# Kernel tuning notes

Measured on AMD Instinct MI355X. Metric: run time of the kernel, lower is better.

Reference implementation:

```python
import jax, jax.numpy as jnp
import numpy as np


def setup_inputs() -> dict:
    key = jax.random.key(0)
    k1, k2, k3 = jax.random.split(key, 3)
    B, Cin, H, W = 32, 128, 56, 56
    E, Cout = 8, 128
    x = jax.random.normal(k1, (B, Cin, H, W), dtype=jnp.float32)
    conv_w = jax.random.normal(k2, (E, Cout, Cin, 3, 3), dtype=jnp.float32) * 0.05
    gate_w = jax.random.normal(k3, (E, Cin), dtype=jnp.float32) * 0.05
    gate_b = jnp.zeros((E,), dtype=jnp.float32)
    return {"x": x, "conv_w": conv_w, "gate_w": gate_w, "gate_b": gate_b, "top_k": 2}


def reference(x, conv_w, gate_w, gate_b, top_k):
    # x: [B, Cin, H, W]; conv_w: [E, Cout, Cin, 3, 3]
    E, Cout, Cin, kh, kw = conv_w.shape
    B = x.shape[0]
    # Gate: global average pool -> linear logits over experts
    gap = x.mean(axis=(2, 3))                      # [B, Cin]
    logits = gap @ gate_w.T + gate_b               # [B, E]
    vals, idx = jax.lax.top_k(logits, top_k)       # [B, k]
    w = jax.nn.softmax(vals, axis=-1)              # renormalize over selected experts
    weights = jnp.zeros((B, E), dtype=x.dtype).at[jnp.arange(B)[:, None], idx].set(w)
    # All experts via a single conv with stacked output channels (stride=1, pad=1 == SAME)
    y = jax.lax.conv_general_dilated(
        x, conv_w.reshape(E * Cout, Cin, kh, kw),
        window_strides=(1, 1), padding='SAME',
        dimension_numbers=('NCHW', 'OIHW', 'NCHW'))  # [B, E*Cout, H, W]
    y = y.reshape(B, E, Cout, y.shape[2], y.shape[3])
    out = jnp.einsum('be,bechw->bchw', weights, y)  # sparse-weight combine
    return out, weights
```

## Files before the change

### kernel.cpp

```cpp
#include <hip/hip_runtime.h>
#include <hip/hip_bf16.h>

constexpr int Bn   = 32;
constexpr int CIN  = 128;
constexpr int Hh   = 56;
constexpr int Ww   = 56;
constexpr int HW   = Hh * Ww;
constexpr int COUT = 128;
constexpr int En   = 8;

typedef __attribute__((ext_vector_type(8))) short bf16x8;
typedef __attribute__((ext_vector_type(4))) float f32x4;

struct GateInfo { int e0, e1; float w0, w1; };

constexpr size_t ROWB = 58 * 64;
constexpr size_t PGB  = 58 * ROWB;
constexpr int TAPSTR  = COUT * CIN;

constexpr size_t XP_OFF  = 0;
constexpr size_t XP_SZ   = (size_t)Bn * 4 * PGB;
constexpr size_t WW_OFF  = XP_OFF + XP_SZ;
constexpr size_t WW_SZ   = (size_t)Bn * 9 * COUT * CIN * 2;
constexpr size_t HS_OFF  = WW_OFF + WW_SZ;
constexpr size_t HS_SZ   = (size_t)Bn * Hh * CIN * 4;
constexpr size_t GAP_OFF = HS_OFF + HS_SZ;
constexpr size_t GAP_SZ  = (size_t)Bn * CIN * 4;
constexpr size_t GI_OFF  = GAP_OFF + GAP_SZ;

__device__ inline void gload_lds16(const void* g, void* l) {
    __builtin_amdgcn_global_load_lds(
        (const __attribute__((address_space(1))) unsigned int*)g,
        (__attribute__((address_space(3))) unsigned int*)l, 16, 0, 0);
}

__global__ __launch_bounds__(256) void convert_kernel(const float* __restrict__ x,
        char* __restrict__ xpad, float* __restrict__ hsum) {
    __shared__ float lt[CIN * 57];
    int gid = blockIdx.x;
    int b = gid / Hh, h = gid % Hh;
    const float* xp = x + (size_t)b * CIN * HW + h * Ww;
    for (int u = threadIdx.x; u < CIN * Ww; u += 256) {
        int c = u / Ww, w = u % Ww;
        lt[c * 57 + w] = xp[(size_t)c * HW + w];
    }
    __syncthreads();
    char* dst = xpad + (size_t)b * 4 * PGB + (size_t)(h + 1) * ROWB;
    for (int u = threadIdx.x; u < 896; u += 256) {
        int g = u / 224, r = u % 224, w = r >> 2, a = r & 3;
        bf16x8 pk;
        #pragma unroll
        for (int j = 0; j < 8; j++) {
            __hip_bfloat16 t = __float2bfloat16(lt[(g * 32 + a * 8 + j) * 57 + w]);
            pk[j] = *reinterpret_cast<short*>(&t);
        }
        int pq = (a + ((w + 1) >> 1)) & 3;
        *(bf16x8*)(dst + (size_t)g * PGB + (size_t)(w + 1) * 64 + pq * 16) = pk;
    }
    if (threadIdx.x < 32) {
        int t = threadIdx.x, g = t >> 3, side = (t >> 2) & 1, q = t & 3;
        *(int4*)(xpad + (size_t)b * 4 * PGB + (size_t)g * PGB + (size_t)(h + 1) * ROWB
                 + (side ? 57 : 0) * 64 + q * 16) = (int4){0, 0, 0, 0};
    }
    if (h == 0 || h == 55) {
        int row = (h == 0) ? 0 : 57;
        char* base = xpad + (size_t)b * 4 * PGB + (size_t)row * ROWB;
        for (int u = threadIdx.x; u < 928; u += 256) {
            int g = u / 232, r = u % 232;
            *(int4*)(base + (size_t)g * PGB + (size_t)r * 16) = (int4){0, 0, 0, 0};
        }
    }
    if (threadIdx.x < CIN) {
        int c = threadIdx.x;
        float s = 0.f;
        #pragma unroll 8
        for (int w = 0; w < Ww; w++) s += lt[c * 57 + w];
        hsum[((size_t)b * Hh + h) * CIN + c] = s;
    }
}

__global__ void gap2_kernel(const float* __restrict__ hsum, float* __restrict__ gap) {
    int t = blockIdx.x * 256 + threadIdx.x;
    int b = t >> 7, c = t & 127;
    float s = 0.f;
    for (int h = 0; h < Hh; h++) s += hsum[((size_t)b * Hh + h) * CIN + c];
    gap[t] = s * (1.f / (float)HW);
}

__global__ void gate_kernel(const float* __restrict__ gap,
                            const float* __restrict__ gate_w,
                            const float* __restrict__ gate_b,
                            float* __restrict__ wout,
                            GateInfo* __restrict__ info) {
    __shared__ float logits[Bn][En];
    __shared__ GateInfo gi[Bn];
    int tid = threadIdx.x;
    int b = tid >> 3, e = tid & 7;
    float s = gate_b[e];
    const float* g = gap + b * CIN;
    const float* w = gate_w + e * CIN;
    #pragma unroll 8
    for (int c = 0; c < CIN; c++) s += g[c] * w[c];
    logits[b][e] = s;
    __syncthreads();
    if (tid < Bn) {
        float v[En];
        #pragma unroll
        for (int k = 0; k < En; k++) v[k] = logits[tid][k];
        int i0 = 0; float m0 = v[0];
        #pragma unroll
        for (int k = 1; k < En; k++) if (v[k] > m0) { m0 = v[k]; i0 = k; }
        int i1 = -1; float m1 = -1e30f;
        #pragma unroll
        for (int k = 0; k < En; k++) if (k != i0 && v[k] > m1) { m1 = v[k]; i1 = k; }
        float ex = expf(m1 - m0);
        float den = 1.f + ex;
        GateInfo t; t.e0 = i0; t.e1 = i1; t.w0 = 1.f / den; t.w1 = ex / den;
        gi[tid] = t;
        info[tid] = t;
    }
    __syncthreads();
    {
        int bb = tid >> 3, ee = tid & 7;
        GateInfo t = gi[bb];
        wout[tid] = (ee == t.e0) ? t.w0 : (ee == t.e1) ? t.w1 : 0.f;
    }
}

__global__ __launch_bounds__(256) void wcomb_kernel(const float* __restrict__ cw,
        const GateInfo* __restrict__ info, __hip_bfloat16* __restrict__ wws) {
    __shared__ __hip_bfloat16 wl[16 * 1152];
    int b = blockIdx.x >> 3, cg = blockIdx.x & 7;
    GateInfo gi = info[b];
    const float* p0 = cw + (size_t)gi.e0 * COUT * CIN * 9 + (size_t)cg * 16 * 1152;
    const float* p1 = cw + (size_t)gi.e1 * COUT * CIN * 9 + (size_t)cg * 16 * 1152;
    for (int u = threadIdx.x; u < 16 * 1152; u += 256)
        wl[u] = __float2bfloat16(gi.w0 * p0[u] + gi.w1 * p1[u]);
    __syncthreads();
    __hip_bfloat16* wo = wws + (size_t)b * 9 * COUT * CIN + (size_t)cg * 16 * CIN;
    for (int u = threadIdx.x; u < 2304; u += 256) {
        int t = u >> 8, rem = u & 255, co = rem >> 4, a = rem & 15;
        bf16x8 pk;
        #pragma unroll
        for (int j = 0; j < 8; j++)
            pk[j] = *reinterpret_cast<short*>(&wl[co * 1152 + (a * 8 + j) * 9 + t]);
        *(bf16x8*)(wo + (size_t)t * COUT * CIN + co * CIN + a * 8) = pk;
    }
}

__global__ __launch_bounds__(256, 2) void conv_mfma(
        const char* __restrict__ xpad,
        const __hip_bfloat16* __restrict__ wws,
        float* __restrict__ out) {
    __shared__ char xs[2][22528];

    int bid = blockIdx.x;
    int xcd = bid & 7, k = bid >> 3;
    int b   = xcd * 4 + k / 14;
    int rb  = k % 14;
    int row0 = rb * 4;
    int tid = threadIdx.x, wave = tid >> 6, lane = tid & 63;
    int cb = wave >> 1, wn = wave & 1;
    int cout0 = cb * 64;
    int l15 = lane & 15, lk = lane >> 4;

    const char* src = xpad + (size_t)b * 4 * PGB + (size_t)row0 * ROWB;

    int bA[7], bB[7], bC[7];
    #pragma unroll
    for (int i = 0; i < 7; i++) {
        int p = wn * 112 + i * 16 + l15;
        int r = p / 56, m = p % 56;
        int base = r * (int)ROWB + m * 64;
        bA[i] = base + ((lk + (m >> 1)) & 3) * 16;
        bB[i] = base + ((lk + (m >> 1) + 1) & 3) * 16;
        bC[i] = (m & 1) ? bB[i] : bA[i];
    }

    const __hip_bfloat16* ap = wws + (size_t)b * 9 * TAPSTR
                             + (size_t)(cout0 + l15) * CIN + lk * 8;

    f32x4 acc[4][7];
    #pragma unroll
    for (int mt = 0; mt < 4; mt++)
        #pragma unroll
        for (int i = 0; i < 7; i++) acc[mt][i] = (f32x4){0.f, 0.f, 0.f, 0.f};

    bf16x8 areg[3][4];
    #pragma unroll
    for (int mt = 0; mt < 4; mt++)
        areg[0][mt] = *(const bf16x8*)(ap + (size_t)0 * TAPSTR + mt * 16 * CIN);
    #pragma unroll
    for (int mt = 0; mt < 4; mt++)
        areg[1][mt] = *(const bf16x8*)(ap + (size_t)1 * TAPSTR + mt * 16 * CIN);

    #pragma unroll
    for (int i = 0; i < 6; i++) {
        int idx = i * 4 + wave;
        if (idx < 22) gload_lds16(src + idx * 1024 + lane * 16, &xs[0][idx * 1024]);
    }

    for (int g = 0; g < 4; ++g) {
        __syncthreads();
        if (g < 3) {
            const char* s2 = src + (size_t)(g + 1) * PGB;
            #pragma unroll
            for (int i = 0; i < 6; i++) {
                int idx = i * 4 + wave;
                if (idx < 22) gload_lds16(s2 + idx * 1024 + lane * 16, &xs[(g + 1) & 1][idx * 1024]);
            }
        }
        const char* xb = xs[g & 1];
        #pragma unroll
        for (int t = 0; t < 9; t++) {
            {
                const int tt = (t < 7) ? t + 2 : t - 7;
                const int gg_add = (t < 7) ? 0 : 1;
                int gg = g + gg_add;
                if (gg < 4) {
                    const __hip_bfloat16* pa = ap + (size_t)tt * TAPSTR + gg * 32;
                    #pragma unroll
                    for (int mt = 0; mt < 4; mt++)
                        areg[(t + 2) % 3][mt] = *(const bf16x8*)(pa + mt * 16 * CIN);
                }
            }
            const int dr = t / 3, dc = t % 3;
            const int imm = dr * (int)ROWB + dc * 64;
            #pragma unroll
            for (int i = 0; i < 7; i++) {
                int boff = (dc == 0) ? bA[i] : (dc == 1) ? bC[i] : bB[i];
                bf16x8 bv = *(const bf16x8*)(xb + boff + imm);
                #pragma unroll
                for (int mt = 0; mt < 4; mt++)
                    acc[mt][i] = __builtin_amdgcn_mfma_f32_16x16x32_bf16(
                        areg[t % 3][mt], bv, acc[mt][i], 0, 0, 0);
            }
        }
    }

    float* outb = out + (size_t)b * COUT * HW + row0 * 56;
    #pragma unroll
    for (int mt = 0; mt < 4; mt++) {
        int cbase = cout0 + mt * 16 + lk * 4;
        #pragma unroll
        for (int i = 0; i < 7; i++) {
            int pp = wn * 112 + i * 16 + l15;
            #pragma unroll
            for (int j = 0; j < 4; j++)
                outb[(size_t)(cbase + j) * HW + pp] = acc[mt][i][j];
        }
    }
}

extern "C" void kernel_launch(void* const* d_in, const int* in_sizes, int n_in,
                              void* d_out, int out_size, void* d_ws, size_t ws_size,
                              hipStream_t stream) {
    const float* x  = (const float*)d_in[0];
    const float* cw = (const float*)d_in[1];
    const float* gw = (const float*)d_in[2];
    const float* gb = (const float*)d_in[3];

    float* out = (float*)d_out;
    char* ws = (char*)d_ws;
    char* xpad           = ws + XP_OFF;
    __hip_bfloat16* wws  = (__hip_bfloat16*)(ws + WW_OFF);
    float* hsum          = (float*)(ws + HS_OFF);
    float* gap           = (float*)(ws + GAP_OFF);
    GateInfo* info       = (GateInfo*)(ws + GI_OFF);
    float* wout = out + (size_t)Bn * COUT * HW;

    convert_kernel<<<Bn * Hh, 256, 0, stream>>>(x, xpad, hsum);
    gap2_kernel   <<<16,      256, 0, stream>>>(hsum, gap);
    gate_kernel   <<<1,       256, 0, stream>>>(gap, gw, gb, wout, info);
    wcomb_kernel  <<<Bn * 8,  256, 0, stream>>>(cw, info, wws);
    conv_mfma     <<<448,     256, 0, stream>>>(xpad, wws, out);
}
```

Before: 170.7 us.

## Double conv tile height to 8 rows with 512 threads; fuse gap and gate kernels

The conv kernel now processes 8 output rows per block with 8 waves (2 cout groups x 4 pixel groups), halving the block count to 224. Each staged input slab covers 10 padded rows, so halo rows are reloaded less often relative to useful work, at the cost of larger LDS buffers and fewer blocks than CUs. Separately, the gap reduction and gating are merged into one per-batch kernel, removing one launch.

Result: no change. 168.4 us (-1.4%).

```diff
diff --git a/kernel.cpp b/kernel.cpp
--- a/kernel.cpp
+++ b/kernel.cpp
@@ -79,34 +79,28 @@
     }
 }
 
-__global__ void gap2_kernel(const float* __restrict__ hsum, float* __restrict__ gap) {
-    int t = blockIdx.x * 256 + threadIdx.x;
-    int b = t >> 7, c = t & 127;
+__global__ __launch_bounds__(128) void gapgate_kernel(const float* __restrict__ hsum,
+        const float* __restrict__ gate_w, const float* __restrict__ gate_b,
+        float* __restrict__ wout, GateInfo* __restrict__ info) {
+    __shared__ float gaps[CIN];
+    __shared__ float lg[En];
+    __shared__ GateInfo gsh;
+    int b = blockIdx.x, tid = threadIdx.x;
     float s = 0.f;
-    for (int h = 0; h < Hh; h++) s += hsum[((size_t)b * Hh + h) * CIN + c];
-    gap[t] = s * (1.f / (float)HW);
-}
-
-__global__ void gate_kernel(const float* __restrict__ gap,
-                            const float* __restrict__ gate_w,
-                            const float* __restrict__ gate_b,
-                            float* __restrict__ wout,
-                            GateInfo* __restrict__ info) {
-    __shared__ float logits[Bn][En];
-    __shared__ GateInfo gi[Bn];
-    int tid = threadIdx.x;
-    int b = tid >> 3, e = tid & 7;
-    float s = gate_b[e];
-    const float* g = gap + b * CIN;
-    const float* w = gate_w + e * CIN;
-    #pragma unroll 8
-    for (int c = 0; c < CIN; c++) s += g[c] * w[c];
-    logits[b][e] = s;
-    __syncthreads();
-    if (tid < Bn) {
+    for (int h = 0; h < Hh; h++) s += hsum[((size_t)b * Hh + h) * CIN + tid];
+    gaps[tid] = s * (1.f / (float)HW);
+    __syncthreads();
+    if (tid < En) {
+        float t = gate_b[tid];
+        #pragma unroll 8
+        for (int c = 0; c < CIN; c++) t += gaps[c] * gate_w[tid * CIN + c];
+        lg[tid] = t;
+    }
+    __syncthreads();
+    if (tid == 0) {
         float v[En];
         #pragma unroll
-        for (int k = 0; k < En; k++) v[k] = logits[tid][k];
+        for (int k = 0; k < En; k++) v[k] = lg[k];
         int i0 = 0; float m0 = v[0];
         #pragma unroll
         for (int k = 1; k < En; k++) if (v[k] > m0) { m0 = v[k]; i0 = k; }
@@ -116,14 +110,12 @@
         float ex = expf(m1 - m0);
         float den = 1.f + ex;
         GateInfo t; t.e0 = i0; t.e1 = i1; t.w0 = 1.f / den; t.w1 = ex / den;
-        gi[tid] = t;
-        info[tid] = t;
-    }
-    __syncthreads();
-    {
-        int bb = tid >> 3, ee = tid & 7;
-        GateInfo t = gi[bb];
-        wout[tid] = (ee == t.e0) ? t.w0 : (ee == t.e1) ? t.w1 : 0.f;
+        gsh = t; info[b] = t;
+    }
+    __syncthreads();
+    if (tid < En) {
+        GateInfo t = gsh;
+        wout[b * En + tid] = (tid == t.e0) ? t.w0 : (tid == t.e1) ? t.w1 : 0.f;
     }
 }
 
@@ -148,19 +140,19 @@
     }
 }
 
-__global__ __launch_bounds__(256, 2) void conv_mfma(
+__global__ __launch_bounds__(512, 2) void conv_mfma(
         const char* __restrict__ xpad,
         const __hip_bfloat16* __restrict__ wws,
         float* __restrict__ out) {
-    __shared__ char xs[2][22528];
+    __shared__ char xs[2][37120];
 
     int bid = blockIdx.x;
     int xcd = bid & 7, k = bid >> 3;
-    int b   = xcd * 4 + k / 14;
-    int rb  = k % 14;
-    int row0 = rb * 4;
+    int b   = xcd * 4 + k / 7;
+    int rb  = k % 7;
+    int row0 = rb * 8;
     int tid = threadIdx.x, wave = tid >> 6, lane = tid & 63;
-    int cb = wave >> 1, wn = wave & 1;
+    int cb = wave >> 2, wq = wave & 3;
     int cout0 = cb * 64;
     int l15 = lane & 15, lk = lane >> 4;
 
@@ -169,7 +161,7 @@
     int bA[7], bB[7], bC[7];
     #pragma unroll
     for (int i = 0; i < 7; i++) {
-        int p = wn * 112 + i * 16 + l15;
+        int p = wq * 112 + i * 16 + l15;
         int r = p / 56, m = p % 56;
         int base = r * (int)ROWB + m * 64;
         bA[i] = base + ((lk + (m >> 1)) & 3) * 16;
@@ -195,9 +187,9 @@
         areg[1][mt] = *(const bf16x8*)(ap + (size_t)1 * TAPSTR + mt * 16 * CIN);
 
     #pragma unroll
-    for (int i = 0; i < 6; i++) {
-        int idx = i * 4 + wave;
-        if (idx < 22) gload_lds16(src + idx * 1024 + lane * 16, &xs[0][idx * 1024]);
+    for (int kk = 0; kk < 5; kk++) {
+        int idx = kk * 512 + tid;
+        if (idx < 2320) gload_lds16(src + (size_t)idx * 16, &xs[0][idx * 16]);
     }
 
     for (int g = 0; g < 4; ++g) {
@@ -205,9 +197,9 @@
         if (g < 3) {
             const char* s2 = src + (size_t)(g + 1) * PGB;
             #pragma unroll
-            for (int i = 0; i < 6; i++) {
-                int idx = i * 4 + wave;
-                if (idx < 22) gload_lds16(s2 + idx * 1024 + lane * 16, &xs[(g + 1) & 1][idx * 1024]);
+            for (int kk = 0; kk < 5; kk++) {
+                int idx = kk * 512 + tid;
+                if (idx < 2320) gload_lds16(s2 + (size_t)idx * 16, &xs[(g + 1) & 1][idx * 16]);
             }
         }
         const char* xb = xs[g & 1];
@@ -244,7 +236,7 @@
         int cbase = cout0 + mt * 16 + lk * 4;
         #pragma unroll
         for (int i = 0; i < 7; i++) {
-            int pp = wn * 112 + i * 16 + l15;
+            int pp = wq * 112 + i * 16 + l15;
             #pragma unroll
             for (int j = 0; j < 4; j++)
                 outb[(size_t)(cbase + j) * HW + pp] = acc[mt][i][j];
@@ -265,13 +257,11 @@
     char* xpad           = ws + XP_OFF;
     __hip_bfloat16* wws  = (__hip_bfloat16*)(ws + WW_OFF);
     float* hsum          = (float*)(ws + HS_OFF);
-    float* gap           = (float*)(ws + GAP_OFF);
     GateInfo* info       = (GateInfo*)(ws + GI_OFF);
     float* wout = out + (size_t)Bn * COUT * HW;
 
     convert_kernel<<<Bn * Hh, 256, 0, stream>>>(x, xpad, hsum);
-    gap2_kernel   <<<16,      256, 0, stream>>>(hsum, gap);
-    gate_kernel   <<<1,       256, 0, stream>>>(gap, gw, gb, wout, info);
+    gapgate_kernel<<<Bn,      128, 0, stream>>>(hsum, gw, gb, wout, info);
     wcomb_kernel  <<<Bn * 8,  256, 0, stream>>>(cw, info, wws);
-    conv_mfma     <<<448,     256, 0, stream>>>(xpad, wws, out);
-}
+    conv_mfma     <<<224,     512, 0, stream>>>(xpad, wws, out);
+}
```
